# Kernel optimization log

Hardware: AMD Instinct MI355X
Metric: run time of the kernel (lower is better)

Reference implementation:

```python
import jax, jax.numpy as jnp
import numpy as np

N_NODES = 10000
N_EDGES = 640000
NODE_DIM = 64
HIDDEN = 128
NUM_LAYERS = 4


def setup_inputs() -> dict:
    key = jax.random.key(0)
    ks = jax.random.split(key, 12)
    s = lambda fan_in: 1.0 / np.sqrt(fan_in)
    inp = {
        'x': jax.random.normal(ks[0], (N_NODES, NODE_DIM), dtype=jnp.float32),
        'edge_index': jax.random.randint(ks[1], (2, N_EDGES), 0, N_NODES, dtype=jnp.int64),
        # node embedding Linear(node_dim, hidden)
        'W_emb': jax.random.uniform(ks[2], (NODE_DIM, HIDDEN), jnp.float32, -s(NODE_DIM), s(NODE_DIM)),
        'b_emb': jnp.zeros((HIDDEN,), jnp.float32),
        # per-layer EdgeConv MLP: Linear(2*hidden, hidden) -> ReLU -> Linear(hidden, hidden)
        'W1': jax.random.uniform(ks[3], (NUM_LAYERS, 2 * HIDDEN, HIDDEN), jnp.float32, -s(2 * HIDDEN), s(2 * HIDDEN)),
        'b1': jnp.zeros((NUM_LAYERS, HIDDEN), jnp.float32),
        'W2': jax.random.uniform(ks[4], (NUM_LAYERS, HIDDEN, HIDDEN), jnp.float32, -s(HIDDEN), s(HIDDEN)),
        'b2': jnp.zeros((NUM_LAYERS, HIDDEN), jnp.float32),
        # final fc Linear(hidden, hidden)
        'W_fc': jax.random.uniform(ks[5], (HIDDEN, HIDDEN), jnp.float32, -s(HIDDEN), s(HIDDEN)),
        'b_fc': jnp.zeros((HIDDEN,), jnp.float32),
    }
    return inp


def _edge_conv(x, src, dst, W1, b1, W2, b2):
    # message: MLP(concat[x_i, x_j - x_i]); x_i = target (dst), x_j = source (src)
    x_i = x[dst]                      # [E, H]
    x_j = x[src]                      # [E, H]
    m = jnp.concatenate([x_i, x_j - x_i], axis=1)  # [E, 2H]
    m = jax.nn.relu(m @ W1 + b1)
    m = m @ W2 + b2                   # [E, H]
    # scatter-max aggregation at target nodes (self loops guarantee coverage)
    return jax.ops.segment_max(m, dst, num_segments=N_NODES)


def reference(x, edge_index, W_emb, b_emb, W1, b1, W2, b2, W_fc, b_fc):
    # add_self_loops
    loops = jnp.arange(N_NODES, dtype=edge_index.dtype)
    src = jnp.concatenate([edge_index[0], loops])
    dst = jnp.concatenate([edge_index[1], loops])

    h = x @ W_emb + b_emb             # [N, H]
    for l in range(NUM_LAYERS):
        h = _edge_conv(h, src, dst, W1[l], b1[l], W2[l], b2[l])
    return h @ W_fc + b_fc
```

## Files before the change

### kernel.cpp

```cpp
#include <hip/hip_runtime.h>

#define N_NODES 10000
#define N_EDGES 640000
#define NODE_DIM 64
#define HIDDEN 128
#define NUM_LAYERS 4
#define NT (N_EDGES + N_NODES)
#define EB8 64

typedef __attribute__((ext_vector_type(8))) short short8v;
typedef __attribute__((ext_vector_type(16))) float f32x16;

__global__ void k_init(const int* __restrict__ ei, int* __restrict__ flag,
                       int* __restrict__ cnt, unsigned int* __restrict__ enc0)
{
    int gid = blockIdx.x * 256 + threadIdx.x;
    if (gid < N_NODES) cnt[gid] = 0;
    for (int i = gid; i < N_NODES * HIDDEN; i += (int)gridDim.x * 256)
        enc0[i] = 0u;
    if (blockIdx.x == 0) {
        __shared__ int nz;
        if (threadIdx.x == 0) nz = 0;
        __syncthreads();
        int found = 0;
        for (int k = threadIdx.x; k < 2048; k += 256) {
            int pos = 2 * (k * 156) + 1;
            if (ei[pos] != 0) found = 1;
        }
        if (found) atomicOr(&nz, 1);
        __syncthreads();
        if (threadIdx.x == 0) flag[0] = nz;
    }
}

__global__ void k_norm_count(const int* __restrict__ ei, const int* __restrict__ flag,
                             int* __restrict__ srcN, int* __restrict__ dstN,
                             int* __restrict__ cnt)
{
    int e = blockIdx.x * 256 + threadIdx.x;
    if (e >= N_EDGES) return;
    int s, d;
    if (flag[0]) { s = ei[e];     d = ei[N_EDGES + e]; }
    else         { s = ei[2 * e]; d = ei[2 * (N_EDGES + e)]; }
    srcN[e] = s;
    dstN[e] = d;
    atomicAdd(&cnt[d], 1);
}

__global__ void k_scan(const int* __restrict__ cnt, int* __restrict__ cursor)
{
    __shared__ int part[256];
    const int t = threadIdx.x;
    const int CH = (N_NODES + 255) / 256;
    int lo = t * CH, hi = min(N_NODES, lo + CH);
    int s = 0;
    for (int i = lo; i < hi; ++i) s += cnt[i] + 1;
    part[t] = s;
    __syncthreads();
    for (int off = 1; off < 256; off <<= 1) {
        int v = (t >= off) ? part[t - off] : 0;
        __syncthreads();
        part[t] += v;
        __syncthreads();
    }
    int base = (t == 0) ? 0 : part[t - 1];
    for (int i = lo; i < hi; ++i) {
        cursor[i] = base;
        base += cnt[i] + 1;
    }
}

__global__ void k_scatter_all(const int* __restrict__ srcN, const int* __restrict__ dstN,
                              int* __restrict__ cursor,
                              int* __restrict__ esrc, int* __restrict__ edst)
{
    int e = blockIdx.x * 256 + threadIdx.x;
    if (e >= NT) return;
    int s, d;
    if (e < N_EDGES) { s = srcN[e]; d = dstN[e]; }
    else             { s = e - N_EDGES; d = s; }
    int pos = atomicAdd(&cursor[d], 1);
    esrc[pos] = s;
    edst[pos] = d;
}

__device__ __forceinline__ unsigned short bf16rne(float f)
{
    unsigned int u = __float_as_uint(f);
    unsigned int r = u + 0x7FFFu + ((u >> 16) & 1u);
    return (unsigned short)(r >> 16);
}

__device__ __forceinline__ void wfrag_store(short* __restrict__ Wf, int k, int n, float w)
{
    unsigned short hs = bf16rne(w);
    float hf = __uint_as_float((unsigned int)hs << 16);
    unsigned short ls = bf16rne(w - hf);
    int c = k >> 4, kh = (k >> 3) & 1, j = k & 7;
    int tile = n >> 5, m = n & 31;
    int lane = kh * 32 + m;
    size_t base = (size_t)c * 4096 + tile * 1024 + lane * 8 + j;
    Wf[base]       = (short)hs;
    Wf[base + 512] = (short)ls;
}

__global__ void k_prepall(const float* __restrict__ W1, const float* __restrict__ W2,
                          const float* __restrict__ W_emb, const float* __restrict__ W_fc,
                          short* __restrict__ Waf, short* __restrict__ Wbf,
                          short* __restrict__ W2f, short* __restrict__ Wembf,
                          short* __restrict__ Wfcf)
{
    int i = blockIdx.x * 256 + threadIdx.x;
    if (i < NUM_LAYERS * 16384) {
        int l = i >> 14, rem = i & 16383;
        int k = rem >> 7, n = rem & 127;
        float top = W1[l * 32768 + rem];
        float bot = W1[l * 32768 + 16384 + rem];
        wfrag_store(Waf + (size_t)l * 32768, k, n, top - bot);
        wfrag_store(Wbf + (size_t)l * 32768, k, n, bot);
        wfrag_store(W2f + (size_t)l * 32768, k, n, W2[i]);
    } else if (i < NUM_LAYERS * 16384 + 8192) {
        int j = i - NUM_LAYERS * 16384;
        wfrag_store(Wembf, j >> 7, j & 127, W_emb[j]);
    } else if (i < NUM_LAYERS * 16384 + 8192 + 16384) {
        int j = i - NUM_LAYERS * 16384 - 8192;
        wfrag_store(Wfcf, j >> 7, j & 127, W_fc[j]);
    }
}

__device__ __forceinline__ unsigned int encf(float f)
{
    unsigned int b = __float_as_uint(f);
    return b ^ ((unsigned int)((int)b >> 31) | 0x80000000u);
}

__device__ __forceinline__ float decenc(unsigned int u)
{
    unsigned int bits = (u & 0x80000000u) ? (u ^ 0x80000000u) : ~u;
    return __uint_as_float(bits);
}

__device__ __forceinline__ void radd_split4(float4 a, float4 b, uint2& H, uint2& L)
{
    float f0 = fmaxf(a.x + b.x, 0.f), f1 = fmaxf(a.y + b.y, 0.f);
    float f2 = fmaxf(a.z + b.z, 0.f), f3 = fmaxf(a.w + b.w, 0.f);
    unsigned int u0 = __float_as_uint(f0), u1 = __float_as_uint(f1);
    unsigned int u2 = __float_as_uint(f2), u3 = __float_as_uint(f3);
    H.x = (u1 & 0xFFFF0000u) | (u0 >> 16);
    H.y = (u3 & 0xFFFF0000u) | (u2 >> 16);
    float r0 = f0 - __uint_as_float(u0 & 0xFFFF0000u);
    float r1 = f1 - __uint_as_float(u1 & 0xFFFF0000u);
    float r2 = f2 - __uint_as_float(u2 & 0xFFFF0000u);
    float r3 = f3 - __uint_as_float(u3 & 0xFFFF0000u);
    L.x = (__float_as_uint(r0) >> 16) | (__float_as_uint(r1) & 0xFFFF0000u);
    L.y = (__float_as_uint(r2) >> 16) | (__float_as_uint(r3) & 0xFFFF0000u);
}

__device__ __forceinline__ void split4_rne(float4 f, uint2& H, uint2& L)
{
    unsigned int h0 = bf16rne(f.x), h1 = bf16rne(f.y);
    unsigned int h2 = bf16rne(f.z), h3 = bf16rne(f.w);
    H.x = h0 | (h1 << 16);
    H.y = h2 | (h3 << 16);
    float r0 = f.x - __uint_as_float(h0 << 16);
    float r1 = f.y - __uint_as_float(h1 << 16);
    float r2 = f.z - __uint_as_float(h2 << 16);
    float r3 = f.w - __uint_as_float(h3 << 16);
    unsigned int l0 = bf16rne(r0), l1 = bf16rne(r1);
    unsigned int l2 = bf16rne(r2), l3 = bf16rne(r3);
    L.x = l0 | (l1 << 16);
    L.y = l2 | (l3 << 16);
}

template <int K, bool HASB, bool DEC>
__global__ __launch_bounds__(256) void k_gemmf(
    const float* __restrict__ Xf, const unsigned int* __restrict__ encR,
    unsigned int* __restrict__ encZ, const float* __restrict__ bprev,
    const short* __restrict__ WAf, const short* __restrict__ WBf,
    const float* __restrict__ biasA,
    float* __restrict__ CA, float* __restrict__ CB, int M)
{
    constexpr int CH = K / 16;
    __shared__ __align__(16) short Ts[4 * CH * 64 * 8];
    const int t = threadIdx.x;
    const int row0 = blockIdx.x * 64;

    {
        const int row = t >> 2, q = t & 3;
        const int gr = row0 + row;
        const int sfrag = row >> 5, mrow = row & 31;
        const int kh = q >> 1, half = q & 1;
        const int lbase = kh * 32 + mrow;
#pragma unroll
        for (int r = 0; r < CH; ++r) {
            float4 v = make_float4(0.f, 0.f, 0.f, 0.f);
            if (gr < M) {
                const int ko = q * 4 + r * 16;
                if constexpr (DEC) {
                    uint4 u = *(const uint4*)(encR + (size_t)gr * K + ko);
                    v.x = decenc(u.x) + bprev[ko + 0];
                    v.y = decenc(u.y) + bprev[ko + 1];
                    v.z = decenc(u.z) + bprev[ko + 2];
                    v.w = decenc(u.w) + bprev[ko + 3];
                    if (encZ)
                        *(uint4*)(encZ + (size_t)gr * K + ko) = make_uint4(0u, 0u, 0u, 0u);
                } else {
                    v = *(const float4*)(Xf + (size_t)gr * K + ko);
                }
            }
            uint2 H, L;
            split4_rne(v, H, L);
            const int c  = r;
            const int ih = ((0 * 2 + sfrag) * CH + c) * 64 + lbase;
            const int il = ((1 * 2 + sfrag) * CH + c) * 64 + lbase;
            *(uint2*)(&Ts[(size_t)(ih ^ c) * 8 + half * 4]) = H;
            *(uint2*)(&Ts[(size_t)(il ^ c) * 8 + half * 4]) = L;
        }
    }
    __syncthreads();

    const int lane = t & 63;
    const int wv   = t >> 6;
    f32x16 aA0 = {0,0,0,0,0,0,0,0,0,0,0,0,0,0,0,0};
    f32x16 aA1 = {0,0,0,0,0,0,0,0,0,0,0,0,0,0,0,0};
    f32x16 aB0 = {0,0,0,0,0,0,0,0,0,0,0,0,0,0,0,0};
    f32x16 aB1 = {0,0,0,0,0,0,0,0,0,0,0,0,0,0,0,0};

    const short* WpA = WAf + (size_t)wv * 1024 + (size_t)lane * 8;
    const short* WpB = HASB ? (WBf + (size_t)wv * 1024 + (size_t)lane * 8) : nullptr;

#pragma unroll
    for (int c = 0; c < CH; ++c) {
        short8v wah = *(const short8v*)(WpA + (size_t)c * 4096);
        short8v wal = *(const short8v*)(WpA + (size_t)c * 4096 + 512);
        short8v ah0 = *(const short8v*)(&Ts[(size_t)((((0 * 2 + 0) * CH + c) * 64 + lane) ^ c) * 8]);
        short8v ah1 = *(const short8v*)(&Ts[(size_t)((((0 * 2 + 1) * CH + c) * 64 + lane) ^ c) * 8]);
        short8v al0 = *(const short8v*)(&Ts[(size_t)((((1 * 2 + 0) * CH + c) * 64 + lane) ^ c) * 8]);
        short8v al1 = *(const short8v*)(&Ts[(size_t)((((1 * 2 + 1) * CH + c) * 64 + lane) ^ c) * 8]);
        aA0 = __builtin_amdgcn_mfma_f32_32x32x16_bf16(ah0, wah, aA0, 0, 0, 0);
        aA0 = __builtin_amdgcn_mfma_f32_32x32x16_bf16(al0, wah, aA0, 0, 0, 0);
        aA0 = __builtin_amdgcn_mfma_f32_32x32x16_bf16(ah0, wal, aA0, 0, 0, 0);
        aA1 = __builtin_amdgcn_mfma_f32_32x32x16_bf16(ah1, wah, aA1, 0, 0, 0);
        aA1 = __builtin_amdgcn_mfma_f32_32x32x16_bf16(al1, wah, aA1, 0, 0, 0);
        aA1 = __builtin_amdgcn_mfma_f32_32x32x16_bf16(ah1, wal, aA1, 0, 0, 0);
        if constexpr (HASB) {
            short8v wbh = *(const short8v*)(WpB + (size_t)c * 4096);
            short8v wbl = *(const short8v*)(WpB + (size_t)c * 4096 + 512);
            aB0 = __builtin_amdgcn_mfma_f32_32x32x16_bf16(ah0, wbh, aB0, 0, 0, 0);
            aB0 = __builtin_amdgcn_mfma_f32_32x32x16_bf16(al0, wbh, aB0, 0, 0, 0);
            aB0 = __builtin_amdgcn_mfma_f32_32x32x16_bf16(ah0, wbl, aB0, 0, 0, 0);
            aB1 = __builtin_amdgcn_mfma_f32_32x32x16_bf16(ah1, wbh, aB1, 0, 0, 0);
            aB1 = __builtin_amdgcn_mfma_f32_32x32x16_bf16(al1, wbh, aB1, 0, 0, 0);
            aB1 = __builtin_amdgcn_mfma_f32_32x32x16_bf16(ah1, wbl, aB1, 0, 0, 0);
        }
    }

    const int m   = lane & 31;
    const int kh  = lane >> 5;
    const int col = wv * 32 + m;
    const float bA = biasA[col];
#pragma unroll
    for (int r = 0; r < 16; ++r) {
        const int er = (r & 3) + 8 * (r >> 2) + 4 * kh;
        const int r0 = row0 + er;
        const int r1 = row0 + 32 + er;
        if (r0 < M) CA[(size_t)r0 * 128 + col] = aA0[r] + bA;
        if (r1 < M) CA[(size_t)r1 * 128 + col] = aA1[r] + bA;
        if constexpr (HASB) {
            if (r0 < M) CB[(size_t)r0 * 128 + col] = aB0[r];
            if (r1 < M) CB[(size_t)r1 * 128 + col] = aB1[r];
        }
    }
}

__global__ __launch_bounds__(256, 4) void k_edge9(
    const float* __restrict__ A, const float* __restrict__ Bm,
    const int* __restrict__ esrc, const int* __restrict__ edst,
    const short* __restrict__ W2l, unsigned int* __restrict__ enc)
{
    __shared__ __align__(16) short Ts[2048 * 8];
    __shared__ int dsts[EB8];

    const int t = threadIdx.x;
    const int lane = t & 63;
    const int wv   = t >> 6;
    const int nwg = (int)gridDim.x;
    const int orig = (int)blockIdx.x;
    const int xcd = orig & 7, idx = orig >> 3;
    const int qq = nwg >> 3, rr = nwg & 7;
    const int bid = (xcd < rr ? xcd * (qq + 1) : rr * (qq + 1) + (xcd - rr) * qq) + idx;
    const int s0 = bid * EB8;

    const short* Wp = W2l + (size_t)wv * 1024 + (size_t)lane * 8;
    short8v bfh[8], bfl[8];
#pragma unroll
    for (int c = 0; c < 8; ++c) {
        bfh[c] = *(const short8v*)(Wp + (size_t)c * 4096);
        bfl[c] = *(const short8v*)(Wp + (size_t)c * 4096 + 512);
    }

    {
        const int row = t >> 2;
        const int q   = t & 3;
        const int slot = s0 + row;
        int dst = -1, src = 0;
        if (slot < NT) { dst = edst[slot]; src = esrc[slot]; }
        if (q == 0) dsts[row] = dst;
        const int sfrag = row >> 5;
        const int mrow  = row & 31;
        const int kh    = q >> 1;
        const int half  = q & 1;
        const int lbase = kh * 32 + mrow;

        if (dst >= 0) {
            const float* Ar = A  + (size_t)dst * HIDDEN + q * 4;
            const float* Br = Bm + (size_t)src * HIDDEN + q * 4;
#pragma unroll
            for (int r = 0; r < 8; ++r) {
                float4 av = *(const float4*)(Ar + r * 16);
                float4 bv = *(const float4*)(Br + r * 16);
                uint2 H, L;
                radd_split4(av, bv, H, L);
                const int c  = r;
                const int ih = ((sfrag)     * 8 + c) * 64 + lbase;
                const int il = ((2 + sfrag) * 8 + c) * 64 + lbase;
                *(uint2*)(&Ts[(size_t)(ih ^ c) * 8 + half * 4]) = H;
                *(uint2*)(&Ts[(size_t)(il ^ c) * 8 + half * 4]) = L;
            }
        } else {
            uint2 z = make_uint2(0u, 0u);
#pragma unroll
            for (int r = 0; r < 8; ++r) {
                const int c  = r;
                const int ih = ((sfrag)     * 8 + c) * 64 + lbase;
                const int il = ((2 + sfrag) * 8 + c) * 64 + lbase;
                *(uint2*)(&Ts[(size_t)(ih ^ c) * 8 + half * 4]) = z;
                *(uint2*)(&Ts[(size_t)(il ^ c) * 8 + half * 4]) = z;
            }
        }
    }
    __syncthreads();

    f32x16 acc0 = {0,0,0,0,0,0,0,0,0,0,0,0,0,0,0,0};
    f32x16 acc1 = {0,0,0,0,0,0,0,0,0,0,0,0,0,0,0,0};

#pragma unroll
    for (int c = 0; c < 8; ++c) {
        short8v ah0 = *(const short8v*)(&Ts[(size_t)(((0 * 8 + c) * 64 + lane) ^ c) * 8]);
        short8v ah1 = *(const short8v*)(&Ts[(size_t)(((1 * 8 + c) * 64 + lane) ^ c) * 8]);
        short8v al0 = *(const short8v*)(&Ts[(size_t)(((2 * 8 + c) * 64 + lane) ^ c) * 8]);
        short8v al1 = *(const short8v*)(&Ts[(size_t)(((3 * 8 + c) * 64 + lane) ^ c) * 8]);
        acc0 = __builtin_amdgcn_mfma_f32_32x32x16_bf16(ah0, bfh[c], acc0, 0, 0, 0);
        acc0 = __builtin_amdgcn_mfma_f32_32x32x16_bf16(al0, bfh[c], acc0, 0, 0, 0);
        acc0 = __builtin_amdgcn_mfma_f32_32x32x16_bf16(ah0, bfl[c], acc0, 0, 0, 0);
        acc1 = __builtin_amdgcn_mfma_f32_32x32x16_bf16(ah1, bfh[c], acc1, 0, 0, 0);
        acc1 = __builtin_amdgcn_mfma_f32_32x32x16_bf16(al1, bfh[c], acc1, 0, 0, 0);
        acc1 = __builtin_amdgcn_mfma_f32_32x32x16_bf16(ah1, bfl[c], acc1, 0, 0, 0);
    }

    const int m   = lane & 31;
    const int kh  = lane >> 5;
    const int col = wv * 32 + m;
    const int d_first = dsts[0];
    const int d_last  = dsts[EB8 - 1];
    if (d_first == d_last) {
        if (d_first >= 0) {
            float mx = fmaxf(acc0[0], acc1[0]);
#pragma unroll
            for (int r = 1; r < 16; ++r)
                mx = fmaxf(mx, fmaxf(acc0[r], acc1[r]));
            atomicMax(&enc[(size_t)d_first * HIDDEN + col], encf(mx));
        }
    } else {
        {
            float run = -3.4e38f;
            int curd = dsts[4 * kh];
#pragma unroll
            for (int r = 0; r < 16; ++r) {
                const int er = (r & 3) + 8 * (r >> 2) + 4 * kh;
                int d = dsts[er];
                if (d != curd) {
                    if (curd >= 0)
                        atomicMax(&enc[(size_t)curd * HIDDEN + col], encf(run));
                    curd = d;
                    run = -3.4e38f;
                }
                run = fmaxf(run, acc0[r]);
            }
            if (curd >= 0)
                atomicMax(&enc[(size_t)curd * HIDDEN + col], encf(run));
        }
        {
            float run = -3.4e38f;
            int curd = dsts[32 + 4 * kh];
#pragma unroll
            for (int r = 0; r < 16; ++r) {
                const int er = 32 + (r & 3) + 8 * (r >> 2) + 4 * kh;
                int d = dsts[er];
                if (d != curd) {
                    if (curd >= 0)
                        atomicMax(&enc[(size_t)curd * HIDDEN + col], encf(run));
                    curd = d;
                    run = -3.4e38f;
                }
                run = fmaxf(run, acc1[r]);
            }
            if (curd >= 0)
                atomicMax(&enc[(size_t)curd * HIDDEN + col], encf(run));
        }
    }
}

extern "C" void kernel_launch(void* const* d_in, const int* in_sizes, int n_in,
                              void* d_out, int out_size, void* d_ws, size_t ws_size,
                              hipStream_t stream)
{
    const float* x     = (const float*)d_in[0];
    const int*   ei    = (const int*)d_in[1];
    const float* W_emb = (const float*)d_in[2];
    const float* b_emb = (const float*)d_in[3];
    const float* W1    = (const float*)d_in[4];
    const float* b1    = (const float*)d_in[5];
    const float* W2    = (const float*)d_in[6];
    const float* b2    = (const float*)d_in[7];
    const float* W_fc  = (const float*)d_in[8];
    const float* b_fc  = (const float*)d_in[9];
    float* out = (float*)d_out;

    char* p = (char*)d_ws;
    auto alloc = [&](size_t bytes) {
        char* r = p;
        p += (bytes + 255) & ~(size_t)255;
        return r;
    };
    float* h    = (float*)alloc((size_t)N_NODES * HIDDEN * 4);
    float* Ab   = (float*)alloc((size_t)N_NODES * HIDDEN * 4);
    float* Bb   = (float*)alloc((size_t)N_NODES * HIDDEN * 4);
    unsigned int* enc0 = (unsigned int*)alloc((size_t)N_NODES * HIDDEN * 4);
    unsigned int* enc1 = (unsigned int*)alloc((size_t)N_NODES * HIDDEN * 4);
    short* Waf  = (short*)alloc((size_t)NUM_LAYERS * 32768 * 2);
    short* Wbf  = (short*)alloc((size_t)NUM_LAYERS * 32768 * 2);
    short* W2f  = (short*)alloc((size_t)NUM_LAYERS * 32768 * 2);
    short* Wembf= (short*)alloc((size_t)16384 * 2);
    short* Wfcf = (short*)alloc((size_t)32768 * 2);
    int* cursor = (int*)alloc(N_NODES * 4);
    int* cnt    = (int*)alloc(N_NODES * 4);
    int* esrc   = (int*)alloc((size_t)NT * 4);
    int* edst   = (int*)alloc((size_t)NT * 4);
    int* srcN   = (int*)alloc((size_t)N_EDGES * 4);
    int* dstN   = (int*)alloc((size_t)N_EDGES * 4);
    int* flag   = (int*)alloc(4);

    unsigned int* encs[2] = {enc0, enc1};

    const int EBLK = (N_EDGES + 255) / 256;
    const int GB   = (N_NODES + 63) / 64;
    const int EG   = (NT + EB8 - 1) / EB8;
    const int PREP = (NUM_LAYERS * 16384 + 8192 + 16384 + 255) / 256;

    k_init<<<(N_NODES * HIDDEN + 255) / 256, 256, 0, stream>>>(ei, flag, cnt, enc0);
    k_norm_count<<<EBLK, 256, 0, stream>>>(ei, flag, srcN, dstN, cnt);
    k_scan<<<1, 256, 0, stream>>>(cnt, cursor);
    k_scatter_all<<<(NT + 255) / 256, 256, 0, stream>>>(srcN, dstN, cursor, esrc, edst);
    k_prepall<<<PREP, 256, 0, stream>>>(W1, W2, W_emb, W_fc, Waf, Wbf, W2f, Wembf, Wfcf);

    k_gemmf<NODE_DIM, false, false><<<GB, 256, 0, stream>>>(
        x, nullptr, nullptr, nullptr, Wembf, nullptr, b_emb, h, nullptr, N_NODES);

    for (int l = 0; l < NUM_LAYERS; ++l) {
        if (l == 0) {
            k_gemmf<HIDDEN, true, false><<<GB, 256, 0, stream>>>(
                h, nullptr, nullptr, nullptr, Waf, Wbf, b1, Ab, Bb, N_NODES);
        } else {
            k_gemmf<HIDDEN, true, true><<<GB, 256, 0, stream>>>(
                nullptr, encs[(l - 1) & 1], encs[l & 1], b2 + (l - 1) * 128,
                Waf + (size_t)l * 32768, Wbf + (size_t)l * 32768,
                b1 + l * 128, Ab, Bb, N_NODES);
        }
        k_edge9<<<EG, 256, 0, stream>>>(Ab, Bb, esrc, edst,
                                        W2f + (size_t)l * 32768, encs[l & 1]);
    }
    k_gemmf<HIDDEN, false, true><<<GB, 256, 0, stream>>>(
        nullptr, encs[(NUM_LAYERS - 1) & 1], nullptr, b2 + 3 * 128,
        Wfcf, nullptr, b_fc, out, nullptr, N_NODES);
}
```

Measured before the change: 502.2 us.

## Halve node-GEMM row tile to 32 and tune edge kernel occupancy and scheduling

The node GEMM kernels now process 32 rows per block instead of 64, which doubles the grid to about 313 blocks and keeps one accumulator pair per wave. The shared-memory staging is rewritten so each thread loads 16 contiguous floats and writes 128-bit LDS stores. The edge kernel's launch-bounds occupancy hint drops from 4 to 3 blocks per SM, and a sched_barrier is added after the weight register preload. The aim is better CU fill for the small node GEMMs and more register headroom in the dominant edge kernel. The cost is that weights are reloaded across twice as many blocks, and the edge kernel may lose some latency hiding.

```diff
diff --git a/kernel.cpp b/kernel.cpp
--- a/kernel.cpp
+++ b/kernel.cpp
@@ -181,77 +181,87 @@
     float* __restrict__ CA, float* __restrict__ CB, int M)
 {
     constexpr int CH = K / 16;
-    __shared__ __align__(16) short Ts[4 * CH * 64 * 8];
+    __shared__ __align__(16) short Ts[2 * CH * 64 * 8];
     const int t = threadIdx.x;
-    const int row0 = blockIdx.x * 64;
+    const int row0 = blockIdx.x * 32;
 
     {
-        const int row = t >> 2, q = t & 3;
-        const int gr = row0 + row;
-        const int sfrag = row >> 5, mrow = row & 31;
-        const int kh = q >> 1, half = q & 1;
-        const int lbase = kh * 32 + mrow;
-#pragma unroll
-        for (int r = 0; r < CH; ++r) {
-            float4 v = make_float4(0.f, 0.f, 0.f, 0.f);
+        const int row = t >> 3;
+        const int c   = t & 7;
+        if (c < CH) {
+            const int gr = row0 + row;
+            float4 a0 = make_float4(0.f,0.f,0.f,0.f), a1 = a0, a2 = a0, a3 = a0;
             if (gr < M) {
-                const int ko = q * 4 + r * 16;
+                const int ko = c * 16;
                 if constexpr (DEC) {
-                    uint4 u = *(const uint4*)(encR + (size_t)gr * K + ko);
-                    v.x = decenc(u.x) + bprev[ko + 0];
-                    v.y = decenc(u.y) + bprev[ko + 1];
-                    v.z = decenc(u.z) + bprev[ko + 2];
-                    v.w = decenc(u.w) + bprev[ko + 3];
-                    if (encZ)
-                        *(uint4*)(encZ + (size_t)gr * K + ko) = make_uint4(0u, 0u, 0u, 0u);
+                    uint4 u0 = *(const uint4*)(encR + (size_t)gr * K + ko);
+                    uint4 u1 = *(const uint4*)(encR + (size_t)gr * K + ko + 4);
+                    uint4 u2 = *(const uint4*)(encR + (size_t)gr * K + ko + 8);
+                    uint4 u3 = *(const uint4*)(encR + (size_t)gr * K + ko + 12);
+                    a0 = make_float4(decenc(u0.x) + bprev[ko+0],  decenc(u0.y) + bprev[ko+1],
+                                     decenc(u0.z) + bprev[ko+2],  decenc(u0.w) + bprev[ko+3]);
+                    a1 = make_float4(decenc(u1.x) + bprev[ko+4],  decenc(u1.y) + bprev[ko+5],
+                                     decenc(u1.z) + bprev[ko+6],  decenc(u1.w) + bprev[ko+7]);
+                    a2 = make_float4(decenc(u2.x) + bprev[ko+8],  decenc(u2.y) + bprev[ko+9],
+                                     decenc(u2.z) + bprev[ko+10], decenc(u2.w) + bprev[ko+11]);
+                    a3 = make_float4(decenc(u3.x) + bprev[ko+12], decenc(u3.y) + bprev[ko+13],
+                                     decenc(u3.z) + bprev[ko+14], decenc(u3.w) + bprev[ko+15]);
+                    if (encZ) {
+                        uint4 z = make_uint4(0u, 0u, 0u, 0u);
+                        *(uint4*)(encZ + (size_t)gr * K + ko)      = z;
+                        *(uint4*)(encZ + (size_t)gr * K + ko + 4)  = z;
+                        *(uint4*)(encZ + (size_t)gr * K + ko + 8)  = z;
+                        *(uint4*)(encZ + (size_t)gr * K + ko + 12) = z;
+                    }
                 } else {
-                    v = *(const float4*)(Xf + (size_t)gr * K + ko);
+                    a0 = *(const float4*)(Xf + (size_t)gr * K + ko);
+                    a1 = *(const float4*)(Xf + (size_t)gr * K + ko + 4);
+                    a2 = *(const float4*)(Xf + (size_t)gr * K + ko + 8);
+                    a3 = *(const float4*)(Xf + (size_t)gr * K + ko + 12);
                 }
             }
-            uint2 H, L;
-            split4_rne(v, H, L);
-            const int c  = r;
-            const int ih = ((0 * 2 + sfrag) * CH + c) * 64 + lbase;
-            const int il = ((1 * 2 + sfrag) * CH + c) * 64 + lbase;
-            *(uint2*)(&Ts[(size_t)(ih ^ c) * 8 + half * 4]) = H;
-            *(uint2*)(&Ts[(size_t)(il ^ c) * 8 + half * 4]) = L;
+            uint2 Ha, La, Hb, Lb;
+            split4_rne(a0, Ha, La); split4_rne(a1, Hb, Lb);
+            uint4 H0 = make_uint4(Ha.x, Ha.y, Hb.x, Hb.y);
+            uint4 L0 = make_uint4(La.x, La.y, Lb.x, Lb.y);
+            split4_rne(a2, Ha, La); split4_rne(a3, Hb, Lb);
+            uint4 H1 = make_uint4(Ha.x, Ha.y, Hb.x, Hb.y);
+            uint4 L1 = make_uint4(La.x, La.y, Lb.x, Lb.y);
+            const int u_h0 = (((0 * CH + c) * 64 +      row) ^ c) * 8;
+            const int u_h1 = (((0 * CH + c) * 64 + 32 + row) ^ c) * 8;
+            const int u_l0 = (((1 * CH + c) * 64 +      row) ^ c) * 8;
+            const int u_l1 = (((1 * CH + c) * 64 + 32 + row) ^ c) * 8;
+            *(uint4*)(&Ts[u_h0]) = H0;
+            *(uint4*)(&Ts[u_h1]) = H1;
+            *(uint4*)(&Ts[u_l0]) = L0;
+            *(uint4*)(&Ts[u_l1]) = L1;
         }
     }
     __syncthreads();
 
     const int lane = t & 63;
     const int wv   = t >> 6;
-    f32x16 aA0 = {0,0,0,0,0,0,0,0,0,0,0,0,0,0,0,0};
-    f32x16 aA1 = {0,0,0,0,0,0,0,0,0,0,0,0,0,0,0,0};
-    f32x16 aB0 = {0,0,0,0,0,0,0,0,0,0,0,0,0,0,0,0};
-    f32x16 aB1 = {0,0,0,0,0,0,0,0,0,0,0,0,0,0,0,0};
+    f32x16 aA = {0,0,0,0,0,0,0,0,0,0,0,0,0,0,0,0};
+    f32x16 aB = {0,0,0,0,0,0,0,0,0,0,0,0,0,0,0,0};
 
     const short* WpA = WAf + (size_t)wv * 1024 + (size_t)lane * 8;
     const short* WpB = HASB ? (WBf + (size_t)wv * 1024 + (size_t)lane * 8) : nullptr;
 
 #pragma unroll
     for (int c = 0; c < CH; ++c) {
+        short8v ah = *(const short8v*)(&Ts[(size_t)((((0 * CH + c) * 64 + lane)) ^ c) * 8]);
+        short8v al = *(const short8v*)(&Ts[(size_t)((((1 * CH + c) * 64 + lane)) ^ c) * 8]);
         short8v wah = *(const short8v*)(WpA + (size_t)c * 4096);
         short8v wal = *(const short8v*)(WpA + (size_t)c * 4096 + 512);
-        short8v ah0 = *(const short8v*)(&Ts[(size_t)((((0 * 2 + 0) * CH + c) * 64 + lane) ^ c) * 8]);
-        short8v ah1 = *(const short8v*)(&Ts[(size_t)((((0 * 2 + 1) * CH + c) * 64 + lane) ^ c) * 8]);
-        short8v al0 = *(const short8v*)(&Ts[(size_t)((((1 * 2 + 0) * CH + c) * 64 + lane) ^ c) * 8]);
-        short8v al1 = *(const short8v*)(&Ts[(size_t)((((1 * 2 + 1) * CH + c) * 64 + lane) ^ c) * 8]);
-        aA0 = __builtin_amdgcn_mfma_f32_32x32x16_bf16(ah0, wah, aA0, 0, 0, 0);
-        aA0 = __builtin_amdgcn_mfma_f32_32x32x16_bf16(al0, wah, aA0, 0, 0, 0);
-        aA0 = __builtin_amdgcn_mfma_f32_32x32x16_bf16(ah0, wal, aA0, 0, 0, 0);
-        aA1 = __builtin_amdgcn_mfma_f32_32x32x16_bf16(ah1, wah, aA1, 0, 0, 0);
-        aA1 = __builtin_amdgcn_mfma_f32_32x32x16_bf16(al1, wah, aA1, 0, 0, 0);
-        aA1 = __builtin_amdgcn_mfma_f32_32x32x16_bf16(ah1, wal, aA1, 0, 0, 0);
+        aA = __builtin_amdgcn_mfma_f32_32x32x16_bf16(ah, wah, aA, 0, 0, 0);
+        aA = __builtin_amdgcn_mfma_f32_32x32x16_bf16(al, wah, aA, 0, 0, 0);
+        aA = __builtin_amdgcn_mfma_f32_32x32x16_bf16(ah, wal, aA, 0, 0, 0);
         if constexpr (HASB) {
             short8v wbh = *(const short8v*)(WpB + (size_t)c * 4096);
             short8v wbl = *(const short8v*)(WpB + (size_t)c * 4096 + 512);
-            aB0 = __builtin_amdgcn_mfma_f32_32x32x16_bf16(ah0, wbh, aB0, 0, 0, 0);
-            aB0 = __builtin_amdgcn_mfma_f32_32x32x16_bf16(al0, wbh, aB0, 0, 0, 0);
-            aB0 = __builtin_amdgcn_mfma_f32_32x32x16_bf16(ah0, wbl, aB0, 0, 0, 0);
-            aB1 = __builtin_amdgcn_mfma_f32_32x32x16_bf16(ah1, wbh, aB1, 0, 0, 0);
-            aB1 = __builtin_amdgcn_mfma_f32_32x32x16_bf16(al1, wbh, aB1, 0, 0, 0);
-            aB1 = __builtin_amdgcn_mfma_f32_32x32x16_bf16(ah1, wbl, aB1, 0, 0, 0);
+            aB = __builtin_amdgcn_mfma_f32_32x32x16_bf16(ah, wbh, aB, 0, 0, 0);
+            aB = __builtin_amdgcn_mfma_f32_32x32x16_bf16(al, wbh, aB, 0, 0, 0);
+            aB = __builtin_amdgcn_mfma_f32_32x32x16_bf16(ah, wbl, aB, 0, 0, 0);
         }
     }
 
@@ -263,17 +273,14 @@
     for (int r = 0; r < 16; ++r) {
         const int er = (r & 3) + 8 * (r >> 2) + 4 * kh;
         const int r0 = row0 + er;
-        const int r1 = row0 + 32 + er;
-        if (r0 < M) CA[(size_t)r0 * 128 + col] = aA0[r] + bA;
-        if (r1 < M) CA[(size_t)r1 * 128 + col] = aA1[r] + bA;
-        if constexpr (HASB) {
-            if (r0 < M) CB[(size_t)r0 * 128 + col] = aB0[r];
-            if (r1 < M) CB[(size_t)r1 * 128 + col] = aB1[r];
-        }
-    }
-}
-
-__global__ __launch_bounds__(256, 4) void k_edge9(
+        if (r0 < M) {
+            CA[(size_t)r0 * 128 + col] = aA[r] + bA;
+            if constexpr (HASB) CB[(size_t)r0 * 128 + col] = aB[r];
+        }
+    }
+}
+
+__global__ __launch_bounds__(256, 3) void k_edge11(
     const float* __restrict__ A, const float* __restrict__ Bm,
     const int* __restrict__ esrc, const int* __restrict__ edst,
     const short* __restrict__ W2l, unsigned int* __restrict__ enc)
@@ -298,6 +305,7 @@
         bfh[c] = *(const short8v*)(Wp + (size_t)c * 4096);
         bfl[c] = *(const short8v*)(Wp + (size_t)c * 4096 + 512);
     }
+    __builtin_amdgcn_sched_barrier(0);
 
     {
         const int row = t >> 2;
@@ -454,7 +462,7 @@
     unsigned int* encs[2] = {enc0, enc1};
 
     const int EBLK = (N_EDGES + 255) / 256;
-    const int GB   = (N_NODES + 63) / 64;
+    const int GB32 = (N_NODES + 31) / 32;
     const int EG   = (NT + EB8 - 1) / EB8;
     const int PREP = (NUM_LAYERS * 16384 + 8192 + 16384 + 255) / 256;
 
@@ -464,23 +472,23 @@
     k_scatter_all<<<(NT + 255) / 256, 256, 0, stream>>>(srcN, dstN, cursor, esrc, edst);
     k_prepall<<<PREP, 256, 0, stream>>>(W1, W2, W_emb, W_fc, Waf, Wbf, W2f, Wembf, Wfcf);
 
-    k_gemmf<NODE_DIM, false, false><<<GB, 256, 0, stream>>>(
+    k_gemmf<NODE_DIM, false, false><<<GB32, 256, 0, stream>>>(
         x, nullptr, nullptr, nullptr, Wembf, nullptr, b_emb, h, nullptr, N_NODES);
 
     for (int l = 0; l < NUM_LAYERS; ++l) {
         if (l == 0) {
-            k_gemmf<HIDDEN, true, false><<<GB, 256, 0, stream>>>(
+            k_gemmf<HIDDEN, true, false><<<GB32, 256, 0, stream>>>(
                 h, nullptr, nullptr, nullptr, Waf, Wbf, b1, Ab, Bb, N_NODES);
         } else {
-            k_gemmf<HIDDEN, true, true><<<GB, 256, 0, stream>>>(
+            k_gemmf<HIDDEN, true, true><<<GB32, 256, 0, stream>>>(
                 nullptr, encs[(l - 1) & 1], encs[l & 1], b2 + (l - 1) * 128,
                 Waf + (size_t)l * 32768, Wbf + (size_t)l * 32768,
                 b1 + l * 128, Ab, Bb, N_NODES);
         }
-        k_edge9<<<EG, 256, 0, stream>>>(Ab, Bb, esrc, edst,
-                                        W2f + (size_t)l * 32768, encs[l & 1]);
-    }
-    k_gemmf<HIDDEN, false, true><<<GB, 256, 0, stream>>>(
+        k_edge11<<<EG, 256, 0, stream>>>(Ab, Bb, esrc, edst,
+                                         W2f + (size_t)l * 32768, encs[l & 1]);
+    }
+    k_gemmf<HIDDEN, false, true><<<GB32, 256, 0, stream>>>(
         nullptr, encs[(NUM_LAYERS - 1) & 1], nullptr, b2 + 3 * 128,
         Wfcf, nullptr, b_fc, out, nullptr, N_NODES);
 }
```

After: 496.4 us. About the same (-1.2%).
